# Optimization experiments

Hardware: AMD Instinct MI355X
Metric: run time of the kernel (lower is better)

Reference implementation:

```python
import jax, jax.numpy as jnp
import numpy as np

N_U, N_D = 7, 7
N_E = N_U + N_D
N_DET = 16
N_FB = 3
N_SV = 256
N_PV = 32
N_A = 2
N_SV_OUT = 3 * N_SV + 2 * N_PV  # 832
N_S_IN = 4 * N_A  # 8
N_P_IN = 4
N_B = 4096
A_POS = np.array([[0.0, 0.0, 0.0], [0.0, 0.0, 1.4]], dtype=np.float32)


def setup_inputs() -> dict:
    key = jax.random.key(0)
    ks = iter(jax.random.split(key, 32))
    w = lambda shape, s=0.05: jax.random.normal(next(ks), shape, jnp.float32) * s
    return {
        'r': jax.random.normal(next(ks), (N_B, N_E, 3), jnp.float32),
        's_w0': w((N_S_IN * 3 + N_P_IN * 2, N_SV)), 's_b0': w((N_SV,)),
        's_w': w((N_FB, N_SV_OUT, N_SV)), 's_b': w((N_FB, N_SV)),
        'p_w0': w((N_P_IN, N_PV)), 'p_b0': w((N_PV,)),
        'p_w': w((N_FB, N_PV, N_PV)), 'p_b': w((N_FB, N_PV)),
        'va_w': w((N_SV_OUT, N_SV)), 'va_b': w((N_SV,)),
        'wu_w': w((N_SV, N_U * N_DET)), 'wu_b': w((N_U * N_DET,)),
        'wd_w': w((N_SV, N_D * N_DET)), 'wd_b': w((N_D * N_DET,)),
        'wf_w': w((N_DET,)),
    }


def fb_block(s_v, p_v):
    # s_v: (b, n_e, ds); p_v: (b, n_e, n_e, dp)
    mu = jnp.broadcast_to(s_v[:, :N_U].mean(axis=1, keepdims=True), s_v.shape)
    md = jnp.broadcast_to(s_v[:, N_U:].mean(axis=1, keepdims=True), s_v.shape)
    pu = p_v[:, :N_U].mean(axis=1)  # (b, n_e, dp)
    pd = p_v[:, N_U:].mean(axis=1)
    return jnp.concatenate([s_v, mu, md, pu, pd], axis=-1)


def _orb(s_x, ra_x, W, b, n_spin):
    nb = s_x.shape[0]
    sw = (s_x @ W + b).reshape(nb, n_spin, n_spin, N_DET)
    env = jnp.exp(-jnp.linalg.norm(ra_x, axis=-1)).sum(axis=-1)[:, :, None, None]
    return jnp.transpose(sw * env, (0, 3, 2, 1))  # (b, n_det, n_spin, n_spin)


def _forward(r, s_w0, s_b0, s_w, s_b, p_w0, p_b0, p_w, p_b, va_w, va_b,
             wu_w, wu_b, wd_w, wd_b, wf_w):
    a = jnp.asarray(A_POS, r.dtype)
    nb = r.shape[0]
    ra = r[:, :, None, :] - a[None, None]  # (b, n_e, n_a, 3)
    ra_len = jnp.linalg.norm(ra, axis=-1, keepdims=True)
    rr = r[:, None, :, :] - r[:, :, None, :]  # (b, n_e, n_e, 3)
    eye = jnp.eye(N_E, dtype=r.dtype)[None, :, :, None]
    rr_len = jnp.linalg.norm(rr + eye, axis=-1, keepdims=True)
    s_v = jnp.concatenate([ra, ra_len], axis=-1).reshape(nb, N_E, -1)  # (b, n_e, 4*n_a)
    p_v = jnp.concatenate([rr, rr_len], axis=-1)  # (b, n_e, n_e, 4)

    ra_u, ra_d = ra[:, :N_U], ra[:, N_U:]

    s_blk = fb_block(s_v, p_v)
    s_v = jnp.tanh(s_blk @ s_w0 + s_b0)
    p_v = jnp.tanh(p_v @ p_w0 + p_b0)
    for i in range(N_FB):
        s_blk = fb_block(s_v, p_v)
        s_v = jnp.tanh(s_blk @ s_w[i] + s_b[i]) + s_v
        p_v = jnp.tanh(p_v @ p_w[i] + p_b[i]) + p_v
    s_blk = fb_block(s_v, p_v)
    s_v = jnp.tanh(s_blk @ va_w + va_b)

    orb_u = _orb(s_v[:, :N_U], ra_u, wu_w, wu_b, N_U)
    orb_d = _orb(s_v[:, N_U:], ra_d, wd_w, wd_b, N_D)
    sign_u, logdet_u = jnp.linalg.slogdet(orb_u)
    sign_d, logdet_d = jnp.linalg.slogdet(orb_d)
    sign = sign_u * sign_d
    logdet = logdet_u + logdet_d  # (b, n_det)
    maxlogdet = jnp.max(logdet, axis=-1, keepdims=True)
    sub_det = sign * jnp.exp(logdet - maxlogdet)
    psi_ish = sub_det @ wf_w  # (b,)
    log_psi = jnp.log(jnp.abs(psi_ish)) + maxlogdet[:, 0]
    return log_psi


def reference(r, s_w0, s_b0, s_w, s_b, p_w0, p_b0, p_w, p_b, va_w, va_b,
              wu_w, wu_b, wd_w, wd_b, wf_w):
    return _forward(r, s_w0, s_b0, s_w, s_b, p_w0, p_b0, p_w, p_b, va_w, va_b,
                    wu_w, wu_b, wd_w, wd_b, wf_w)
```

## Files before the change

kernel.cpp:

```cpp
#include <hip/hip_runtime.h>
#include <math.h>

#define N_U 7
#define N_E 14
#define N_DET 16
#define N_FB 3
#define N_SV 256
#define N_PV 32
#define N_PAIR 196

__device__ __forceinline__ float tanh_fast(float x) {
    float e = __expf(2.0f * x);
    return 1.0f - __fdividef(2.0f, e + 1.0f);
}

union SharedU {
    struct { float sblk0[N_E][32]; float pin[N_PAIR][4]; } a;
    float orb[2 * N_DET][49];
};

extern "C" __global__ void __launch_bounds__(256, 3)
ansatz_kernel(const float* __restrict__ r_g,
              const float* __restrict__ s_w0, const float* __restrict__ s_b0,
              const float* __restrict__ s_w,  const float* __restrict__ s_b,
              const float* __restrict__ p_w0, const float* __restrict__ p_b0,
              const float* __restrict__ p_w,  const float* __restrict__ p_b,
              const float* __restrict__ va_w, const float* __restrict__ va_b,
              const float* __restrict__ wu_w, const float* __restrict__ wu_b,
              const float* __restrict__ wd_w, const float* __restrict__ wd_b,
              const float* __restrict__ wf_w, float* __restrict__ out)
{
    const int bid = blockIdx.x;
    const int nwg = gridDim.x;
    const int b = ((nwg & 7) == 0) ? ((bid & 7) * (nwg >> 3) + (bid >> 3)) : bid;
    const int t = threadIdx.x;

    __shared__ float sv[N_E][N_SV];
    __shared__ float pv[N_PAIR][N_PV];
    __shared__ float mu_s[N_SV], md_s[N_SV];
    __shared__ float pu_s[N_E][N_PV], pd_s[N_E][N_PV];
    __shared__ SharedU su;
    __shared__ float envs[N_E];
    __shared__ float rbuf[N_E * 3];
    __shared__ float dsg[2 * N_DET], dld[2 * N_DET];

    if (t < N_E * 3) rbuf[t] = r_g[b * N_E * 3 + t];
    __syncthreads();

    if (t < N_E) {
        float rx = rbuf[t * 3], ry = rbuf[t * 3 + 1], rz = rbuf[t * 3 + 2];
        float l0 = sqrtf(rx * rx + ry * ry + rz * rz);
        float z1 = rz - 1.4f;
        float l1 = sqrtf(rx * rx + ry * ry + z1 * z1);
        su.a.sblk0[t][0] = rx; su.a.sblk0[t][1] = ry; su.a.sblk0[t][2] = rz; su.a.sblk0[t][3] = l0;
        su.a.sblk0[t][4] = rx; su.a.sblk0[t][5] = ry; su.a.sblk0[t][6] = z1; su.a.sblk0[t][7] = l1;
        envs[t] = __expf(-l0) + __expf(-l1);
    }
    if (t < N_PAIR) {
        int i = t / N_E, j = t % N_E;
        float dx = rbuf[j * 3 + 0] - rbuf[i * 3 + 0];
        float dy = rbuf[j * 3 + 1] - rbuf[i * 3 + 1];
        float dz = rbuf[j * 3 + 2] - rbuf[i * 3 + 2];
        float ee = (i == j) ? 1.0f : 0.0f;
        float lx = dx + ee, ly = dy + ee, lz = dz + ee;
        float len = sqrtf(lx * lx + ly * ly + lz * lz);
        su.a.pin[t][0] = dx; su.a.pin[t][1] = dy; su.a.pin[t][2] = dz; su.a.pin[t][3] = len;
    }
    __syncthreads();

    if (t < 112) {
        int e = t / 8, k = t % 8;
        float su_ = 0.f, sd_ = 0.f;
        for (int i = 0; i < 7; i++)  su_ += su.a.sblk0[i][k];
        for (int i = 7; i < 14; i++) sd_ += su.a.sblk0[i][k];
        su.a.sblk0[e][8 + k]  = su_ * (1.f / 7.f);
        su.a.sblk0[e][16 + k] = sd_ * (1.f / 7.f);
    }
    if (t >= 128 && t < 128 + 56) {
        int q = t - 128; int j = q / 4, c = q % 4;
        float su_ = 0.f, sd_ = 0.f;
        for (int i = 0; i < 7; i++)  su_ += su.a.pin[i * N_E + j][c];
        for (int i = 7; i < 14; i++) sd_ += su.a.pin[i * N_E + j][c];
        su.a.sblk0[j][24 + c] = su_ * (1.f / 7.f);
        su.a.sblk0[j][28 + c] = sd_ * (1.f / 7.f);
    }
    __syncthreads();

    {
        const int n = t;
        float acc[N_E];
        float bias = s_b0[n];
        #pragma unroll
        for (int e = 0; e < N_E; e++) acc[e] = bias;
        for (int k = 0; k < 32; k += 4) {
            float w0 = s_w0[(k + 0) * N_SV + n];
            float w1 = s_w0[(k + 1) * N_SV + n];
            float w2 = s_w0[(k + 2) * N_SV + n];
            float w3 = s_w0[(k + 3) * N_SV + n];
            #pragma unroll
            for (int e = 0; e < N_E; e++) {
                float4 s4 = *(const float4*)&su.a.sblk0[e][k];
                acc[e] += s4.x * w0 + s4.y * w1 + s4.z * w2 + s4.w * w3;
            }
        }
        #pragma unroll
        for (int e = 0; e < N_E; e++) sv[e][n] = tanh_fast(acc[e]);
    }

    {
        const int c = t & 31, pr0 = t >> 5;
        float w0 = p_w0[c], w1 = p_w0[32 + c], w2 = p_w0[64 + c], w3 = p_w0[96 + c];
        float bias = p_b0[c];
        #pragma unroll
        for (int m = 0; m < 25; m++) {
            int pair = pr0 + (m << 3);
            if (pair < N_PAIR) {
                float4 q4 = *(const float4*)&su.a.pin[pair][0];
                pv[pair][c] = tanh_fast(bias + q4.x * w0 + q4.y * w1 + q4.z * w2 + q4.w * w3);
            }
        }
    }
    __syncthreads();

    for (int it = 0; it <= N_FB; it++) {
        {
            const int n = t;
            float su_ = 0.f, sd_ = 0.f;
            #pragma unroll
            for (int e = 0; e < 7; e++)  su_ += sv[e][n];
            #pragma unroll
            for (int e = 7; e < 14; e++) sd_ += sv[e][n];
            mu_s[n] = su_ * (1.f / 7.f);
            md_s[n] = sd_ * (1.f / 7.f);
        }
        for (int idx = t; idx < N_E * N_PV; idx += 256) {
            int j = idx >> 5, c = idx & 31;
            float su_ = 0.f, sd_ = 0.f;
            for (int i = 0; i < 7; i++)  su_ += pv[i * N_E + j][c];
            for (int i = 7; i < 14; i++) sd_ += pv[i * N_E + j][c];
            pu_s[j][c] = su_ * (1.f / 7.f);
            pd_s[j][c] = sd_ * (1.f / 7.f);
        }
        __syncthreads();

        const bool last = (it == N_FB);
        const float* W = last ? va_w : (s_w + it * 832 * N_SV);
        const float* B = last ? va_b : (s_b + it * N_SV);
        const int n = t;

        float base = B[n];
        #pragma unroll 2
        for (int k = 0; k < N_SV; k += 4) {
            float4 m4 = *(const float4*)&mu_s[k];
            const float* Wk = W + (N_SV + k) * N_SV + n;
            base += m4.x * Wk[0] + m4.y * Wk[N_SV] + m4.z * Wk[2 * N_SV] + m4.w * Wk[3 * N_SV];
            float4 d4 = *(const float4*)&md_s[k];
            const float* Wk2 = W + (2 * N_SV + k) * N_SV + n;
            base += d4.x * Wk2[0] + d4.y * Wk2[N_SV] + d4.z * Wk2[2 * N_SV] + d4.w * Wk2[3 * N_SV];
        }

        float acc[N_E];
        #pragma unroll
        for (int e = 0; e < N_E; e++) acc[e] = base;

        #pragma unroll 2
        for (int k = 0; k < N_SV; k += 4) {
            const float* Wk = W + k * N_SV + n;
            float w0 = Wk[0], w1 = Wk[N_SV], w2 = Wk[2 * N_SV], w3 = Wk[3 * N_SV];
            #pragma unroll
            for (int e = 0; e < N_E; e++) {
                float4 s4 = *(const float4*)&sv[e][k];
                acc[e] += s4.x * w0 + s4.y * w1 + s4.z * w2 + s4.w * w3;
            }
        }
        for (int k = 0; k < N_PV; k += 4) {
            const float* Wk = W + (3 * N_SV + k) * N_SV + n;
            float w0 = Wk[0], w1 = Wk[N_SV], w2 = Wk[2 * N_SV], w3 = Wk[3 * N_SV];
            #pragma unroll
            for (int e = 0; e < N_E; e++) {
                float4 q4 = *(const float4*)&pu_s[e][k];
                acc[e] += q4.x * w0 + q4.y * w1 + q4.z * w2 + q4.w * w3;
            }
            const float* Wk2 = W + (3 * N_SV + N_PV + k) * N_SV + n;
            float v0 = Wk2[0], v1 = Wk2[N_SV], v2 = Wk2[2 * N_SV], v3 = Wk2[3 * N_SV];
            #pragma unroll
            for (int e = 0; e < N_E; e++) {
                float4 q4 = *(const float4*)&pd_s[e][k];
                acc[e] += q4.x * v0 + q4.y * v1 + q4.z * v2 + q4.w * v3;
            }
        }

        #pragma unroll
        for (int e = 0; e < N_E; e++) {
            float th = tanh_fast(acc[e]);
            acc[e] = last ? th : (th + sv[e][n]);
        }
        __syncthreads();
        #pragma unroll
        for (int e = 0; e < N_E; e++) sv[e][n] = acc[e];
        __syncthreads();

        if (!last) {
            const int c = t & 31, pr0 = t >> 5;
            float wreg[N_PV];
            #pragma unroll
            for (int k = 0; k < N_PV; k++) wreg[k] = p_w[it * N_PV * N_PV + k * N_PV + c];
            const float bias = p_b[it * N_PV + c];

            #pragma unroll
            for (int ch = 0; ch < 2; ch++) {
                const int pbase = ch * 98;
                float res[13];
                #pragma unroll
                for (int m = 0; m < 13; m++) {
                    int q = pr0 + (m << 3);
                    if (q < 98) {
                        int pair = pbase + q;
                        float a = bias;
                        #pragma unroll
                        for (int k = 0; k < N_PV; k += 4) {
                            float4 q4 = *(const float4*)&pv[pair][k];
                            a += q4.x * wreg[k] + q4.y * wreg[k + 1] + q4.z * wreg[k + 2] + q4.w * wreg[k + 3];
                        }
                        res[m] = tanh_fast(a) + pv[pair][c];
                    }
                }
                __syncthreads();
                #pragma unroll
                for (int m = 0; m < 13; m++) {
                    int q = pr0 + (m << 3);
                    if (q < 98) pv[pbase + q][c] = res[m];
                }
                __syncthreads();
            }
        }
    }

    for (int idx = t; idx < 2 * 784; idx += 256) {
        int sgrp = idx / 784;
        int rem  = idx % 784;
        int e    = rem / 112;
        int col  = rem % 112;
        const float* W  = sgrp ? wd_w : wu_w;
        const float* Bb = sgrp ? wd_b : wu_b;
        float a = Bb[col];
        const float* srow = sv[sgrp * 7 + e];
        for (int k = 0; k < N_SV; k += 4) {
            float4 s4 = *(const float4*)&srow[k];
            a += s4.x * W[(k + 0) * 112 + col] + s4.y * W[(k + 1) * 112 + col]
               + s4.z * W[(k + 2) * 112 + col] + s4.w * W[(k + 3) * 112 + col];
        }
        int o = col / 16, d = col % 16;
        su.orb[sgrp * 16 + d][o * 7 + e] = a * envs[sgrp * 7 + e];
    }
    __syncthreads();

    if (t < 32) {
        float* A = su.orb[t];
        float sg = 1.0f, ld = 0.0f;
        for (int c0 = 0; c0 < 7; c0++) {
            int p = c0; float mx = fabsf(A[c0 * 7 + c0]);
            for (int rI = c0 + 1; rI < 7; rI++) {
                float v = fabsf(A[rI * 7 + c0]);
                if (v > mx) { mx = v; p = rI; }
            }
            if (p != c0) {
                for (int c2 = 0; c2 < 7; c2++) {
                    float tmp = A[c0 * 7 + c2]; A[c0 * 7 + c2] = A[p * 7 + c2]; A[p * 7 + c2] = tmp;
                }
                sg = -sg;
            }
            float piv = A[c0 * 7 + c0];
            if (piv < 0.f) sg = -sg;
            ld += __logf(fabsf(piv));
            float rp = 1.0f / piv;
            for (int rI = c0 + 1; rI < 7; rI++) {
                float f = A[rI * 7 + c0] * rp;
                for (int c2 = c0 + 1; c2 < 7; c2++) A[rI * 7 + c2] -= f * A[c0 * 7 + c2];
            }
        }
        dsg[t] = sg; dld[t] = ld;
    }
    __syncthreads();

    if (t == 0) {
        float mx = -1e30f;
        float ld[16], sg[16];
        #pragma unroll
        for (int d = 0; d < 16; d++) {
            ld[d] = dld[d] + dld[16 + d];
            sg[d] = dsg[d] * dsg[16 + d];
            mx = fmaxf(mx, ld[d]);
        }
        float psi = 0.f;
        #pragma unroll
        for (int d = 0; d < 16; d++) psi += sg[d] * __expf(ld[d] - mx) * wf_w[d];
        out[b] = __logf(fabsf(psi)) + mx;
    }
}

extern "C" void kernel_launch(void* const* d_in, const int* in_sizes, int n_in,
                              void* d_out, int out_size, void* d_ws, size_t ws_size,
                              hipStream_t stream) {
    (void)n_in; (void)d_ws; (void)ws_size; (void)out_size;
    const float* r    = (const float*)d_in[0];
    const float* s_w0 = (const float*)d_in[1];
    const float* s_b0 = (const float*)d_in[2];
    const float* s_w  = (const float*)d_in[3];
    const float* s_b  = (const float*)d_in[4];
    const float* p_w0 = (const float*)d_in[5];
    const float* p_b0 = (const float*)d_in[6];
    const float* p_w  = (const float*)d_in[7];
    const float* p_b  = (const float*)d_in[8];
    const float* va_w = (const float*)d_in[9];
    const float* va_b = (const float*)d_in[10];
    const float* wu_w = (const float*)d_in[11];
    const float* wu_b = (const float*)d_in[12];
    const float* wd_w = (const float*)d_in[13];
    const float* wd_b = (const float*)d_in[14];
    const float* wf_w = (const float*)d_in[15];
    float* out = (float*)d_out;

    const int nb = in_sizes[0] / (N_E * 3);
    hipLaunchKernelGGL(ansatz_kernel, dim3(nb), dim3(256), 0, stream,
                       r, s_w0, s_b0, s_w, s_b, p_w0, p_b0, p_w, p_b,
                       va_w, va_b, wu_w, wu_b, wd_w, wd_b, wf_w, out);
}
```

Baseline: 2.586 ms.

## Process two samples per 512-thread workgroup with dynamic shared memory

Result: slower. 7.954 ms (+207.6%).

```diff
diff --git a/kernel.cpp b/kernel.cpp
--- a/kernel.cpp
+++ b/kernel.cpp
@@ -9,17 +9,31 @@
 #define N_PV 32
 #define N_PAIR 196
 
+#define F_SV   3584
+#define F_PV   6272
+#define F_MU   256
+#define F_PUPD 448
+#define F_SU   1568
+#define OFF_SV   0
+#define OFF_PV   (OFF_SV + 2*F_SV)
+#define OFF_MU   (OFF_PV + 2*F_PV)
+#define OFF_MD   (OFF_MU + 2*F_MU)
+#define OFF_PU   (OFF_MD + 2*F_MU)
+#define OFF_PD   (OFF_PU + 2*F_PUPD)
+#define OFF_SU   (OFF_PD + 2*F_PUPD)
+#define OFF_ENV  (OFF_SU + 2*F_SU)
+#define OFF_RB   (OFF_ENV + 2*16)
+#define OFF_DSG  (OFF_RB + 2*48)
+#define OFF_DLD  (OFF_DSG + 2*32)
+#define LDS_FLOATS (OFF_DLD + 2*32)
+#define LDS_BYTES  (LDS_FLOATS * 4)
+
 __device__ __forceinline__ float tanh_fast(float x) {
     float e = __expf(2.0f * x);
     return 1.0f - __fdividef(2.0f, e + 1.0f);
 }
 
-union SharedU {
-    struct { float sblk0[N_E][32]; float pin[N_PAIR][4]; } a;
-    float orb[2 * N_DET][49];
-};
-
-extern "C" __global__ void __launch_bounds__(256, 3)
+extern "C" __global__ void __launch_bounds__(512, 1)
 ansatz_kernel(const float* __restrict__ r_g,
               const float* __restrict__ s_w0, const float* __restrict__ s_b0,
               const float* __restrict__ s_w,  const float* __restrict__ s_b,
@@ -30,64 +44,74 @@
               const float* __restrict__ wd_w, const float* __restrict__ wd_b,
               const float* __restrict__ wf_w, float* __restrict__ out)
 {
+    extern __shared__ float lds[];
+
     const int bid = blockIdx.x;
     const int nwg = gridDim.x;
-    const int b = ((nwg & 7) == 0) ? ((bid & 7) * (nwg >> 3) + (bid >> 3)) : bid;
-    const int t = threadIdx.x;
-
-    __shared__ float sv[N_E][N_SV];
-    __shared__ float pv[N_PAIR][N_PV];
-    __shared__ float mu_s[N_SV], md_s[N_SV];
-    __shared__ float pu_s[N_E][N_PV], pd_s[N_E][N_PV];
-    __shared__ SharedU su;
-    __shared__ float envs[N_E];
-    __shared__ float rbuf[N_E * 3];
-    __shared__ float dsg[2 * N_DET], dld[2 * N_DET];
-
-    if (t < N_E * 3) rbuf[t] = r_g[b * N_E * 3 + t];
-    __syncthreads();
-
-    if (t < N_E) {
-        float rx = rbuf[t * 3], ry = rbuf[t * 3 + 1], rz = rbuf[t * 3 + 2];
+    const int bsw = ((nwg & 7) == 0) ? ((bid & 7) * (nwg >> 3) + (bid >> 3)) : bid;
+    const int t  = threadIdx.x;
+    const int h  = t >> 8;
+    const int tl = t & 255;
+    const int b2 = 2 * bsw + h;
+
+    float* svp  = lds + OFF_SV  + h * F_SV;
+    float* pvp  = lds + OFF_PV  + h * F_PV;
+    float* mu   = lds + OFF_MU  + h * F_MU;
+    float* md   = lds + OFF_MD  + h * F_MU;
+    float* pu   = lds + OFF_PU  + h * F_PUPD;
+    float* pd   = lds + OFF_PD  + h * F_PUPD;
+    float* sb   = lds + OFF_SU  + h * F_SU;
+    float* env  = lds + OFF_ENV + h * 16;
+    float* rb   = lds + OFF_RB  + h * 48;
+    float* dsgp = lds + OFF_DSG + h * 32;
+    float* dldp = lds + OFF_DLD + h * 32;
+
+    if (tl < N_E * 3) rb[tl] = r_g[b2 * N_E * 3 + tl];
+    __syncthreads();
+
+    if (tl < N_E) {
+        float rx = rb[tl * 3], ry = rb[tl * 3 + 1], rz = rb[tl * 3 + 2];
         float l0 = sqrtf(rx * rx + ry * ry + rz * rz);
         float z1 = rz - 1.4f;
         float l1 = sqrtf(rx * rx + ry * ry + z1 * z1);
-        su.a.sblk0[t][0] = rx; su.a.sblk0[t][1] = ry; su.a.sblk0[t][2] = rz; su.a.sblk0[t][3] = l0;
-        su.a.sblk0[t][4] = rx; su.a.sblk0[t][5] = ry; su.a.sblk0[t][6] = z1; su.a.sblk0[t][7] = l1;
-        envs[t] = __expf(-l0) + __expf(-l1);
-    }
-    if (t < N_PAIR) {
-        int i = t / N_E, j = t % N_E;
-        float dx = rbuf[j * 3 + 0] - rbuf[i * 3 + 0];
-        float dy = rbuf[j * 3 + 1] - rbuf[i * 3 + 1];
-        float dz = rbuf[j * 3 + 2] - rbuf[i * 3 + 2];
+        float* s0 = sb + tl * 32;
+        s0[0] = rx; s0[1] = ry; s0[2] = rz; s0[3] = l0;
+        s0[4] = rx; s0[5] = ry; s0[6] = z1; s0[7] = l1;
+        env[tl] = __expf(-l0) + __expf(-l1);
+    }
+    if (tl < N_PAIR) {
+        int i = tl / N_E, j = tl % N_E;
+        float dx = rb[j * 3 + 0] - rb[i * 3 + 0];
+        float dy = rb[j * 3 + 1] - rb[i * 3 + 1];
+        float dz = rb[j * 3 + 2] - rb[i * 3 + 2];
         float ee = (i == j) ? 1.0f : 0.0f;
         float lx = dx + ee, ly = dy + ee, lz = dz + ee;
         float len = sqrtf(lx * lx + ly * ly + lz * lz);
-        su.a.pin[t][0] = dx; su.a.pin[t][1] = dy; su.a.pin[t][2] = dz; su.a.pin[t][3] = len;
-    }
-    __syncthreads();
-
-    if (t < 112) {
-        int e = t / 8, k = t % 8;
+        float* pn = sb + 448 + tl * 4;
+        pn[0] = dx; pn[1] = dy; pn[2] = dz; pn[3] = len;
+    }
+    __syncthreads();
+
+    if (tl < 112) {
+        int e = tl / 8, k = tl % 8;
         float su_ = 0.f, sd_ = 0.f;
-        for (int i = 0; i < 7; i++)  su_ += su.a.sblk0[i][k];
-        for (int i = 7; i < 14; i++) sd_ += su.a.sblk0[i][k];
-        su.a.sblk0[e][8 + k]  = su_ * (1.f / 7.f);
-        su.a.sblk0[e][16 + k] = sd_ * (1.f / 7.f);
-    }
-    if (t >= 128 && t < 128 + 56) {
-        int q = t - 128; int j = q / 4, c = q % 4;
+        for (int i = 0; i < 7; i++)  su_ += sb[i * 32 + k];
+        for (int i = 7; i < 14; i++) sd_ += sb[i * 32 + k];
+        sb[e * 32 + 8 + k]  = su_ * (1.f / 7.f);
+        sb[e * 32 + 16 + k] = sd_ * (1.f / 7.f);
+    }
+    if (tl >= 128 && tl < 128 + 56) {
+        int q = tl - 128; int j = q / 4, c = q % 4;
         float su_ = 0.f, sd_ = 0.f;
-        for (int i = 0; i < 7; i++)  su_ += su.a.pin[i * N_E + j][c];
-        for (int i = 7; i < 14; i++) sd_ += su.a.pin[i * N_E + j][c];
-        su.a.sblk0[j][24 + c] = su_ * (1.f / 7.f);
-        su.a.sblk0[j][28 + c] = sd_ * (1.f / 7.f);
+        for (int i = 0; i < 7; i++)  su_ += sb[448 + (i * N_E + j) * 4 + c];
+        for (int i = 7; i < 14; i++) sd_ += sb[448 + (i * N_E + j) * 4 + c];
+        sb[j * 32 + 24 + c] = su_ * (1.f / 7.f);
+        sb[j * 32 + 28 + c] = sd_ * (1.f / 7.f);
     }
     __syncthreads();
 
     {
-        const int n = t;
+        const int n = tl;
         float acc[N_E];
         float bias = s_b0[n];
         #pragma unroll
@@ -99,24 +123,24 @@
             float w3 = s_w0[(k + 3) * N_SV + n];
             #pragma unroll
             for (int e = 0; e < N_E; e++) {
-                float4 s4 = *(const float4*)&su.a.sblk0[e][k];
+                float4 s4 = *(const float4*)&sb[e * 32 + k];
                 acc[e] += s4.x * w0 + s4.y * w1 + s4.z * w2 + s4.w * w3;
             }
         }
         #pragma unroll
-        for (int e = 0; e < N_E; e++) sv[e][n] = tanh_fast(acc[e]);
+        for (int e = 0; e < N_E; e++) svp[e * N_SV + n] = tanh_fast(acc[e]);
     }
 
     {
-        const int c = t & 31, pr0 = t >> 5;
+        const int c = tl & 31, pr0 = tl >> 5;
         float w0 = p_w0[c], w1 = p_w0[32 + c], w2 = p_w0[64 + c], w3 = p_w0[96 + c];
         float bias = p_b0[c];
         #pragma unroll
         for (int m = 0; m < 25; m++) {
             int pair = pr0 + (m << 3);
             if (pair < N_PAIR) {
-                float4 q4 = *(const float4*)&su.a.pin[pair][0];
-                pv[pair][c] = tanh_fast(bias + q4.x * w0 + q4.y * w1 + q4.z * w2 + q4.w * w3);
+                float4 q4 = *(const float4*)&sb[448 + pair * 4];
+                pvp[pair * N_PV + c] = tanh_fast(bias + q4.x * w0 + q4.y * w1 + q4.z * w2 + q4.w * w3);
             }
         }
     }
@@ -124,37 +148,37 @@
 
     for (int it = 0; it <= N_FB; it++) {
         {
-            const int n = t;
+            const int n = tl;
             float su_ = 0.f, sd_ = 0.f;
             #pragma unroll
-            for (int e = 0; e < 7; e++)  su_ += sv[e][n];
-            #pragma unroll
-            for (int e = 7; e < 14; e++) sd_ += sv[e][n];
-            mu_s[n] = su_ * (1.f / 7.f);
-            md_s[n] = sd_ * (1.f / 7.f);
-        }
-        for (int idx = t; idx < N_E * N_PV; idx += 256) {
+            for (int e = 0; e < 7; e++)  su_ += svp[e * N_SV + n];
+            #pragma unroll
+            for (int e = 7; e < 14; e++) sd_ += svp[e * N_SV + n];
+            mu[n] = su_ * (1.f / 7.f);
+            md[n] = sd_ * (1.f / 7.f);
+        }
+        for (int idx = tl; idx < N_E * N_PV; idx += 256) {
             int j = idx >> 5, c = idx & 31;
             float su_ = 0.f, sd_ = 0.f;
-            for (int i = 0; i < 7; i++)  su_ += pv[i * N_E + j][c];
-            for (int i = 7; i < 14; i++) sd_ += pv[i * N_E + j][c];
-            pu_s[j][c] = su_ * (1.f / 7.f);
-            pd_s[j][c] = sd_ * (1.f / 7.f);
+            for (int i = 0; i < 7; i++)  su_ += pvp[(i * N_E + j) * N_PV + c];
+            for (int i = 7; i < 14; i++) sd_ += pvp[(i * N_E + j) * N_PV + c];
+            pu[j * N_PV + c] = su_ * (1.f / 7.f);
+            pd[j * N_PV + c] = sd_ * (1.f / 7.f);
         }
         __syncthreads();
 
         const bool last = (it == N_FB);
         const float* W = last ? va_w : (s_w + it * 832 * N_SV);
         const float* B = last ? va_b : (s_b + it * N_SV);
-        const int n = t;
+        const int n = tl;
 
         float base = B[n];
         #pragma unroll 2
         for (int k = 0; k < N_SV; k += 4) {
-            float4 m4 = *(const float4*)&mu_s[k];
+            float4 m4 = *(const float4*)&mu[k];
             const float* Wk = W + (N_SV + k) * N_SV + n;
             base += m4.x * Wk[0] + m4.y * Wk[N_SV] + m4.z * Wk[2 * N_SV] + m4.w * Wk[3 * N_SV];
-            float4 d4 = *(const float4*)&md_s[k];
+            float4 d4 = *(const float4*)&md[k];
             const float* Wk2 = W + (2 * N_SV + k) * N_SV + n;
             base += d4.x * Wk2[0] + d4.y * Wk2[N_SV] + d4.z * Wk2[2 * N_SV] + d4.w * Wk2[3 * N_SV];
         }
@@ -169,7 +193,7 @@
             float w0 = Wk[0], w1 = Wk[N_SV], w2 = Wk[2 * N_SV], w3 = Wk[3 * N_SV];
             #pragma unroll
             for (int e = 0; e < N_E; e++) {
-                float4 s4 = *(const float4*)&sv[e][k];
+                float4 s4 = *(const float4*)&svp[e * N_SV + k];
                 acc[e] += s4.x * w0 + s4.y * w1 + s4.z * w2 + s4.w * w3;
             }
         }
@@ -178,14 +202,14 @@
             float w0 = Wk[0], w1 = Wk[N_SV], w2 = Wk[2 * N_SV], w3 = Wk[3 * N_SV];
             #pragma unroll
             for (int e = 0; e < N_E; e++) {
-                float4 q4 = *(const float4*)&pu_s[e][k];
+                float4 q4 = *(const float4*)&pu[e * N_PV + k];
                 acc[e] += q4.x * w0 + q4.y * w1 + q4.z * w2 + q4.w * w3;
             }
             const float* Wk2 = W + (3 * N_SV + N_PV + k) * N_SV + n;
             float v0 = Wk2[0], v1 = Wk2[N_SV], v2 = Wk2[2 * N_SV], v3 = Wk2[3 * N_SV];
             #pragma unroll
             for (int e = 0; e < N_E; e++) {
-                float4 q4 = *(const float4*)&pd_s[e][k];
+                float4 q4 = *(const float4*)&pd[e * N_PV + k];
                 acc[e] += q4.x * v0 + q4.y * v1 + q4.z * v2 + q4.w * v3;
             }
         }
@@ -193,15 +217,15 @@
         #pragma unroll
         for (int e = 0; e < N_E; e++) {
             float th = tanh_fast(acc[e]);
-            acc[e] = last ? th : (th + sv[e][n]);
+            acc[e] = last ? th : (th + svp[e * N_SV + n]);
         }
         __syncthreads();
         #pragma unroll
-        for (int e = 0; e < N_E; e++) sv[e][n] = acc[e];
+        for (int e = 0; e < N_E; e++) svp[e * N_SV + n] = acc[e];
         __syncthreads();
 
         if (!last) {
-            const int c = t & 31, pr0 = t >> 5;
+            const int c = tl & 31, pr0 = tl >> 5;
             float wreg[N_PV];
             #pragma unroll
             for (int k = 0; k < N_PV; k++) wreg[k] = p_w[it * N_PV * N_PV + k * N_PV + c];
@@ -219,24 +243,24 @@
                         float a = bias;
                         #pragma unroll
                         for (int k = 0; k < N_PV; k += 4) {
-                            float4 q4 = *(const float4*)&pv[pair][k];
+                            float4 q4 = *(const float4*)&pvp[pair * N_PV + k];
                             a += q4.x * wreg[k] + q4.y * wreg[k + 1] + q4.z * wreg[k + 2] + q4.w * wreg[k + 3];
                         }
-                        res[m] = tanh_fast(a) + pv[pair][c];
+                        res[m] = tanh_fast(a) + pvp[pair * N_PV + c];
                     }
                 }
                 __syncthreads();
                 #pragma unroll
                 for (int m = 0; m < 13; m++) {
                     int q = pr0 + (m << 3);
-                    if (q < 98) pv[pbase + q][c] = res[m];
+                    if (q < 98) pvp[(pbase + q) * N_PV + c] = res[m];
                 }
                 __syncthreads();
             }
         }
     }
 
-    for (int idx = t; idx < 2 * 784; idx += 256) {
+    for (int idx = tl; idx < 2 * 784; idx += 256) {
         int sgrp = idx / 784;
         int rem  = idx % 784;
         int e    = rem / 112;
@@ -244,19 +268,19 @@
         const float* W  = sgrp ? wd_w : wu_w;
         const float* Bb = sgrp ? wd_b : wu_b;
         float a = Bb[col];
-        const float* srow = sv[sgrp * 7 + e];
+        const float* srow = svp + (sgrp * 7 + e) * N_SV;
         for (int k = 0; k < N_SV; k += 4) {
             float4 s4 = *(const float4*)&srow[k];
             a += s4.x * W[(k + 0) * 112 + col] + s4.y * W[(k + 1) * 112 + col]
                + s4.z * W[(k + 2) * 112 + col] + s4.w * W[(k + 3) * 112 + col];
         }
         int o = col / 16, d = col % 16;
-        su.orb[sgrp * 16 + d][o * 7 + e] = a * envs[sgrp * 7 + e];
-    }
-    __syncthreads();
-
-    if (t < 32) {
-        float* A = su.orb[t];
+        sb[(sgrp * 16 + d) * 49 + o * 7 + e] = a * env[sgrp * 7 + e];
+    }
+    __syncthreads();
+
+    if (tl < 32) {
+        float* A = sb + tl * 49;
         float sg = 1.0f, ld = 0.0f;
         for (int c0 = 0; c0 < 7; c0++) {
             int p = c0; float mx = fabsf(A[c0 * 7 + c0]);
@@ -279,23 +303,23 @@
                 for (int c2 = c0 + 1; c2 < 7; c2++) A[rI * 7 + c2] -= f * A[c0 * 7 + c2];
             }
         }
-        dsg[t] = sg; dld[t] = ld;
-    }
-    __syncthreads();
-
-    if (t == 0) {
+        dsgp[tl] = sg; dldp[tl] = ld;
+    }
+    __syncthreads();
+
+    if (tl == 0) {
         float mx = -1e30f;
         float ld[16], sg[16];
         #pragma unroll
         for (int d = 0; d < 16; d++) {
-            ld[d] = dld[d] + dld[16 + d];
-            sg[d] = dsg[d] * dsg[16 + d];
+            ld[d] = dldp[d] + dldp[16 + d];
+            sg[d] = dsgp[d] * dsgp[16 + d];
             mx = fmaxf(mx, ld[d]);
         }
         float psi = 0.f;
         #pragma unroll
         for (int d = 0; d < 16; d++) psi += sg[d] * __expf(ld[d] - mx) * wf_w[d];
-        out[b] = __logf(fabsf(psi)) + mx;
+        out[b2] = __logf(fabsf(psi)) + mx;
     }
 }
 
@@ -321,8 +345,11 @@
     const float* wf_w = (const float*)d_in[15];
     float* out = (float*)d_out;
 
+    hipFuncSetAttribute((const void*)ansatz_kernel,
+                        hipFuncAttributeMaxDynamicSharedMemorySize, LDS_BYTES);
+
     const int nb = in_sizes[0] / (N_E * 3);
-    hipLaunchKernelGGL(ansatz_kernel, dim3(nb), dim3(256), 0, stream,
+    hipLaunchKernelGGL(ansatz_kernel, dim3(nb / 2), dim3(512), LDS_BYTES, stream,
                        r, s_w0, s_b0, s_w, s_b, p_w0, p_b0, p_w, p_b,
                        va_w, va_b, wu_w, wu_b, wd_w, wd_b, wf_w, out);
 }
```
